# Kernel optimization log

Measured on AMD Instinct MI355X. Metric: run time of the kernel, lower is better.

Reference implementation:

```python
import jax, jax.numpy as jnp
import numpy as np

NUM_EXPERTS = 8
TOP_K = 2
HIDDEN = 2048
INTER = 1024
B, S = 4, 1024


def setup_inputs() -> dict:
    key = jax.random.key(0)
    ks = jax.random.split(key, 5)
    sx = 1.0 / np.sqrt(HIDDEN)
    si = 1.0 / np.sqrt(INTER)
    return {
        "x": jax.random.normal(ks[0], (B, S, HIDDEN), dtype=jnp.float32),
        # router gate: Linear(hidden -> num_experts), weight stored [E, H] (torch convention)
        "gate_w": jax.random.normal(ks[1], (NUM_EXPERTS, HIDDEN), dtype=jnp.float32) * sx,
        # stacked expert weights: gate/up [E, I, H], down [E, H, I]
        "gate_proj_w": jax.random.normal(ks[2], (NUM_EXPERTS, INTER, HIDDEN), dtype=jnp.float32) * sx,
        "up_proj_w": jax.random.normal(ks[3], (NUM_EXPERTS, INTER, HIDDEN), dtype=jnp.float32) * sx,
        "down_proj_w": jax.random.normal(ks[4], (NUM_EXPERTS, HIDDEN, INTER), dtype=jnp.float32) * si,
    }


def _moe_forward(x, gate_w, gate_proj_w, up_proj_w, down_proj_w):
    Bx, Sx, H = x.shape
    T = Bx * Sx
    h = x.reshape(T, H)
    # --- routing (Qwen3: softmax in fp32, top-k, renormalize) ---
    router_logits = h @ gate_w.T                                   # [T, E]
    probs = jax.nn.softmax(router_logits.astype(jnp.float32), axis=-1)
    top_vals, top_idx = jax.lax.top_k(probs, TOP_K)                # [T, K]
    top_vals = top_vals / jnp.sum(top_vals, axis=-1, keepdims=True)  # norm_topk_prob
    # dense routing weights [T, E]: zero for unselected experts
    rw = jnp.zeros((T, NUM_EXPERTS), dtype=jnp.float32)
    rw = rw.at[jnp.arange(T)[:, None], top_idx].add(top_vals)
    rw = rw.astype(h.dtype)
    # --- SwiGLU experts, computed densely and masked by routing weights ---
    g = jnp.einsum('th,eih->tei', h, gate_proj_w)                  # [T, E, I]
    u = jnp.einsum('th,eih->tei', h, up_proj_w)                    # [T, E, I]
    a = jax.nn.silu(g) * u                                         # [T, E, I]
    out_e = jnp.einsum('tei,ehi->teh', a, down_proj_w)             # [T, E, H]
    out = jnp.einsum('te,teh->th', rw, out_e)                      # [T, H]
    return out.reshape(Bx, Sx, H)


def reference(x, gate_w, gate_proj_w, up_proj_w, down_proj_w):
    return _moe_forward(x, gate_w, gate_proj_w, up_proj_w, down_proj_w)
```

## Files before the change

### kernel.cpp

```cpp
#include <hip/hip_runtime.h>
#include <hip/hip_bf16.h>

#define NUM_EXPERTS 8
#define HIDDEN 2048
#define INTER 1024
#define T_TOKENS 4096

#define BK 32
#define GU_BM 64
#define GU_BN 128
#define DN_BM 64
#define DN_BN 128

typedef __attribute__((ext_vector_type(8))) short short8;
typedef __attribute__((ext_vector_type(4))) float f32x4;

__device__ __forceinline__ ushort f2bf(float f) {
    __hip_bfloat16 h = __float2bfloat16(f);
    return *reinterpret_cast<ushort*>(&h);
}

__device__ __forceinline__ void load_lds16(const void* g, void* lds) {
    __builtin_amdgcn_global_load_lds(
        (const __attribute__((address_space(1))) void*)g,
        (__attribute__((address_space(3))) void*)lds, 16, 0, 0);
}

__global__ __launch_bounds__(256) void cvt_bf16(const float* __restrict__ in,
                                                ushort* __restrict__ out, int n4) {
    int i = blockIdx.x * 256 + threadIdx.x;
    int stride = gridDim.x * 256;
    for (; i < n4; i += stride) {
        float4 v = reinterpret_cast<const float4*>(in)[i];
        ushort4 o;
        o.x = f2bf(v.x); o.y = f2bf(v.y); o.z = f2bf(v.z); o.w = f2bf(v.w);
        reinterpret_cast<ushort4*>(out)[i] = o;
    }
}

__global__ __launch_bounds__(256) void moe_router(const float* __restrict__ x,
                                                  const float* __restrict__ gw,
                                                  int* __restrict__ top_idx,
                                                  float* __restrict__ top_w,
                                                  int* __restrict__ counts) {
    int wid = threadIdx.x >> 6;
    int lane = threadIdx.x & 63;
    int t = blockIdx.x * 4 + wid;
    if (t >= T_TOKENS) return;
    const float* xt = x + (size_t)t * HIDDEN;
    float acc[NUM_EXPERTS];
#pragma unroll
    for (int e = 0; e < NUM_EXPERTS; e++) acc[e] = 0.f;
    for (int h = lane; h < HIDDEN; h += 64) {
        float xv = xt[h];
#pragma unroll
        for (int e = 0; e < NUM_EXPERTS; e++)
            acc[e] = fmaf(xv, gw[e * HIDDEN + h], acc[e]);
    }
#pragma unroll
    for (int e = 0; e < NUM_EXPERTS; e++) {
#pragma unroll
        for (int off = 32; off > 0; off >>= 1)
            acc[e] += __shfl_xor(acc[e], off);
    }
    if (lane == 0) {
        int i1 = 0; float l1 = acc[0];
#pragma unroll
        for (int e = 1; e < NUM_EXPERTS; e++)
            if (acc[e] > l1) { l1 = acc[e]; i1 = e; }
        int i2 = -1; float l2 = -3.4e38f;
#pragma unroll
        for (int e = 0; e < NUM_EXPERTS; e++)
            if (e != i1 && acc[e] > l2) { l2 = acc[e]; i2 = e; }
        float w2 = __expf(l2 - l1);
        float denom = 1.f + w2;
        top_idx[t * 2 + 0] = i1;
        top_idx[t * 2 + 1] = i2;
        top_w[t * 2 + 0] = 1.f / denom;
        top_w[t * 2 + 1] = w2 / denom;
        atomicAdd(&counts[i1], 1);
        atomicAdd(&counts[i2], 1);
    }
}

__global__ void moe_offsets(const int* __restrict__ counts,
                            int* __restrict__ ebase, int* __restrict__ cursor) {
    if (threadIdx.x == 0 && blockIdx.x == 0) {
        int s = 0;
        for (int e = 0; e < NUM_EXPERTS; e++) {
            ebase[e] = s; cursor[e] = s; s += counts[e];
        }
    }
}

__global__ __launch_bounds__(256) void moe_scatter(const int* __restrict__ top_idx,
                                                   const float* __restrict__ top_w,
                                                   int* __restrict__ cursor,
                                                   int* __restrict__ slot_tok,
                                                   float* __restrict__ slot_w) {
    int t = blockIdx.x * 256 + threadIdx.x;
    if (t >= T_TOKENS) return;
#pragma unroll
    for (int k = 0; k < 2; k++) {
        int e = top_idx[t * 2 + k];
        int pos = atomicAdd(&cursor[e], 1);
        slot_tok[pos] = t;
        slot_w[pos] = top_w[t * 2 + k];
    }
}

__global__ __launch_bounds__(256, 4) void moe_gateup(const ushort* __restrict__ xb,
                                                     const ushort* __restrict__ wgb,
                                                     const ushort* __restrict__ wub,
                                                     const int* __restrict__ slot_tok,
                                                     const int* __restrict__ ebase,
                                                     const int* __restrict__ ecnt,
                                                     ushort* __restrict__ act) {
    __shared__ ushort ldsA[2][GU_BM * BK];
    __shared__ ushort ldsG[2][GU_BN * BK];
    __shared__ ushort ldsU[2][GU_BN * BK];

    const int wg = blockIdx.x;
    const int wgid = (wg & 7) * 512 + (wg >> 3);
    const int e = wgid >> 9;
    const int rem = wgid & 511;
    const int bm = rem & 63;
    const int bn = rem >> 6;

    const int cnt = ecnt[e];
    if (bm * GU_BM >= cnt) return;
    const int b0 = ebase[e];

    const int tid = threadIdx.x;
    const int lane = tid & 63;
    const int wid = tid >> 6;
    const int wr = wid >> 1, wc = wid & 1;

    const int r = tid >> 2, cs = tid & 3;
    const int scl = (cs ^ ((r >> 1) & 3)) * 8;
    const int ar = bm * GU_BM + r;
    const int tok = slot_tok[b0 + ((ar < cnt) ? ar : (cnt - 1))];
    const ushort* pA = xb + (size_t)tok * HIDDEN + scl;
    const size_t wrow0 = (size_t)e * INTER + (size_t)(bn * GU_BN + r);
    const ushort* pG0 = wgb + wrow0 * HIDDEN + scl;
    const ushort* pG1 = pG0 + (size_t)64 * HIDDEN;
    const ushort* pU0 = wub + wrow0 * HIDDEN + scl;
    const ushort* pU1 = pU0 + (size_t)64 * HIDDEN;

    const int fr = lane & 15;
    const int colsw = (((lane >> 4) ^ ((fr >> 1) & 3)) * 8);

    f32x4 accg[2][4] = {};
    f32x4 accu[2][4] = {};

#define GU_STAGE(buf, t)                                              \
    do {                                                              \
        const int _o = (t) * BK;                                      \
        load_lds16(pA + _o,  &ldsA[buf][tid * 8]);                    \
        load_lds16(pG0 + _o, &ldsG[buf][tid * 8]);                    \
        load_lds16(pG1 + _o, &ldsG[buf][2048 + tid * 8]);             \
        load_lds16(pU0 + _o, &ldsU[buf][tid * 8]);                    \
        load_lds16(pU1 + _o, &ldsU[buf][2048 + tid * 8]);             \
    } while (0)

#define GU_FRAGS_MFMA(cur)                                            \
    do {                                                              \
        const ushort* LA = ldsA[cur];                                 \
        const ushort* LG = ldsG[cur];                                 \
        const ushort* LU = ldsU[cur];                                 \
        short8 a[2], bg[4], bu[4];                                    \
        _Pragma("unroll")                                             \
        for (int m = 0; m < 2; m++)                                   \
            a[m] = *(const short8*)(LA + (wr * 32 + m * 16 + fr) * BK + colsw); \
        _Pragma("unroll")                                             \
        for (int n = 0; n < 4; n++) {                                 \
            bg[n] = *(const short8*)(LG + (wc * 64 + n * 16 + fr) * BK + colsw); \
            bu[n] = *(const short8*)(LU + (wc * 64 + n * 16 + fr) * BK + colsw); \
        }                                                             \
        asm volatile("s_waitcnt lgkmcnt(0)" ::: "memory");            \
        asm volatile("s_barrier" ::: "memory");                       \
        if (t + 2 < NT) GU_STAGE(cur, t + 2);                         \
        _Pragma("unroll")                                             \
        for (int m = 0; m < 2; m++) {                                 \
            _Pragma("unroll")                                         \
            for (int n = 0; n < 4; n++) {                             \
                accg[m][n] = __builtin_amdgcn_mfma_f32_16x16x32_bf16(a[m], bg[n], accg[m][n], 0, 0, 0); \
                accu[m][n] = __builtin_amdgcn_mfma_f32_16x16x32_bf16(a[m], bu[n], accu[m][n], 0, 0, 0); \
            }                                                         \
        }                                                             \
    } while (0)

    const int NT = HIDDEN / BK;
    GU_STAGE(0, 0);
    GU_STAGE(1, 1);

    for (int t = 0; t < NT - 1; ++t) {
        asm volatile("s_waitcnt vmcnt(5)" ::: "memory");
        asm volatile("s_barrier" ::: "memory");
        const int cur = t & 1;
        GU_FRAGS_MFMA(cur);
    }
    {
        const int t = NT - 1;
        asm volatile("s_waitcnt vmcnt(0)" ::: "memory");
        asm volatile("s_barrier" ::: "memory");
        const int cur = t & 1;
        GU_FRAGS_MFMA(cur);
    }
#undef GU_FRAGS_MFMA
#undef GU_STAGE

#pragma unroll
    for (int m = 0; m < 2; m++) {
#pragma unroll
        for (int rr = 0; rr < 4; rr++) {
            int row = bm * GU_BM + wr * 32 + m * 16 + (lane >> 4) * 4 + rr;
            if (row < cnt) {
                size_t arow = (size_t)(b0 + row) * INTER;
#pragma unroll
                for (int n = 0; n < 4; n++) {
                    int col = bn * GU_BN + wc * 64 + n * 16 + fr;
                    float g = accg[m][n][rr];
                    float u = accu[m][n][rr];
                    float s = g / (1.f + __expf(-g));
                    act[arow + col] = f2bf(s * u);
                }
            }
        }
    }
}

__global__ __launch_bounds__(256, 6) void moe_down(const ushort* __restrict__ act,
                                                   const ushort* __restrict__ wdb,
                                                   const int* __restrict__ slot_tok,
                                                   const float* __restrict__ slot_w,
                                                   const int* __restrict__ ebase,
                                                   const int* __restrict__ ecnt,
                                                   float* __restrict__ out) {
    __shared__ ushort ldsA[2][DN_BM * BK];
    __shared__ ushort ldsB[2][DN_BN * BK];

    const int wg = blockIdx.x;
    const int wgid = (wg & 7) * 1024 + (wg >> 3);
    const int e = wgid >> 10;
    const int rem = wgid & 1023;
    const int bm = rem & 63;
    const int bn = rem >> 6;

    const int cnt = ecnt[e];
    if (bm * DN_BM >= cnt) return;
    const int b0 = ebase[e];

    const int tid = threadIdx.x;
    const int lane = tid & 63;
    const int wid = tid >> 6;
    const int wr = wid >> 1, wc = wid & 1;

    const int r = tid >> 2, cs = tid & 3;
    const int scl = (cs ^ ((r >> 1) & 3)) * 8;
    const int ar = bm * DN_BM + r;
    const int sr = b0 + ((ar < cnt) ? ar : (cnt - 1));
    const ushort* pA = act + (size_t)sr * INTER + scl;
    const size_t wrow = (size_t)e * HIDDEN + (size_t)(bn * DN_BN + r);
    const ushort* pB0 = wdb + wrow * INTER + scl;
    const ushort* pB1 = pB0 + (size_t)64 * INTER;

    const int fr = lane & 15;
    const int colsw = (((lane >> 4) ^ ((fr >> 1) & 3)) * 8);

    f32x4 acc[2][4] = {};

#define DN_STAGE(buf, t)                                              \
    do {                                                              \
        const int _o = (t) * BK;                                      \
        load_lds16(pA + _o,  &ldsA[buf][tid * 8]);                    \
        load_lds16(pB0 + _o, &ldsB[buf][tid * 8]);                    \
        load_lds16(pB1 + _o, &ldsB[buf][2048 + tid * 8]);             \
    } while (0)

#define DN_FRAGS_MFMA(cur)                                            \
    do {                                                              \
        const ushort* LA = ldsA[cur];                                 \
        const ushort* LB = ldsB[cur];                                 \
        short8 a[2], b[4];                                            \
        _Pragma("unroll")                                             \
        for (int m = 0; m < 2; m++)                                   \
            a[m] = *(const short8*)(LA + (wr * 32 + m * 16 + fr) * BK + colsw); \
        _Pragma("unroll")                                             \
        for (int n = 0; n < 4; n++)                                   \
            b[n] = *(const short8*)(LB + (wc * 64 + n * 16 + fr) * BK + colsw); \
        asm volatile("s_waitcnt lgkmcnt(0)" ::: "memory");            \
        asm volatile("s_barrier" ::: "memory");                       \
        if (t + 2 < NT) DN_STAGE(cur, t + 2);                         \
        _Pragma("unroll")                                             \
        for (int m = 0; m < 2; m++) {                                 \
            _Pragma("unroll")                                         \
            for (int n = 0; n < 4; n++)                               \
                acc[m][n] = __builtin_amdgcn_mfma_f32_16x16x32_bf16(a[m], b[n], acc[m][n], 0, 0, 0); \
        }                                                             \
    } while (0)

    const int NT = INTER / BK;
    DN_STAGE(0, 0);
    DN_STAGE(1, 1);

    for (int t = 0; t < NT - 1; ++t) {
        asm volatile("s_waitcnt vmcnt(3)" ::: "memory");
        asm volatile("s_barrier" ::: "memory");
        const int cur = t & 1;
        DN_FRAGS_MFMA(cur);
    }
    {
        const int t = NT - 1;
        asm volatile("s_waitcnt vmcnt(0)" ::: "memory");
        asm volatile("s_barrier" ::: "memory");
        const int cur = t & 1;
        DN_FRAGS_MFMA(cur);
    }
#undef DN_FRAGS_MFMA
#undef DN_STAGE

#pragma unroll
    for (int m = 0; m < 2; m++) {
#pragma unroll
        for (int rr = 0; rr < 4; rr++) {
            int row = bm * DN_BM + wr * 32 + m * 16 + (lane >> 4) * 4 + rr;
            if (row < cnt) {
                int slot = b0 + row;
                int tok = slot_tok[slot];
                float w = slot_w[slot];
                float* orow = out + (size_t)tok * HIDDEN;
#pragma unroll
                for (int n = 0; n < 4; n++) {
                    int col = bn * DN_BN + wc * 64 + n * 16 + fr;
                    atomicAdd(&orow[col], acc[m][n][rr] * w);
                }
            }
        }
    }
}

extern "C" void kernel_launch(void* const* d_in, const int* in_sizes, int n_in,
                              void* d_out, int out_size, void* d_ws, size_t ws_size,
                              hipStream_t stream) {
    const float* x  = (const float*)d_in[0];
    const float* gw = (const float*)d_in[1];
    const float* wg = (const float*)d_in[2];
    const float* wu = (const float*)d_in[3];
    const float* wd = (const float*)d_in[4];
    float* out = (float*)d_out;

    char* ws = (char*)d_ws;
    ushort* xb  = (ushort*)(ws);
    ushort* wgb = (ushort*)(ws + 16777216);
    ushort* wub = (ushort*)(ws + 16777216 + 33554432);
    ushort* wdb = (ushort*)(ws + 16777216 + 2u * 33554432);
    ushort* act = (ushort*)(ws + 16777216 + 3u * 33554432);
    char* p = ws + 2u * 16777216 + 3u * 33554432;
    int*   top_idx  = (int*)p;   p += 32768;
    float* top_w    = (float*)p; p += 32768;
    int*   slot_tok = (int*)p;   p += 32768;
    float* slot_w   = (float*)p; p += 32768;
    int*   counts   = (int*)p;   p += 128;
    int*   ebase    = (int*)p;   p += 128;
    int*   cursor   = (int*)p;   p += 128;

    hipMemsetAsync(counts, 0, 128, stream);
    hipMemsetAsync(d_out, 0, (size_t)out_size * sizeof(float), stream);

    cvt_bf16<<<1024, 256, 0, stream>>>(x,  xb,  (T_TOKENS * HIDDEN) / 4);
    cvt_bf16<<<1024, 256, 0, stream>>>(wg, wgb, (NUM_EXPERTS * INTER * HIDDEN) / 4);
    cvt_bf16<<<1024, 256, 0, stream>>>(wu, wub, (NUM_EXPERTS * INTER * HIDDEN) / 4);
    cvt_bf16<<<1024, 256, 0, stream>>>(wd, wdb, (NUM_EXPERTS * HIDDEN * INTER) / 4);

    moe_router<<<T_TOKENS / 4, 256, 0, stream>>>(x, gw, top_idx, top_w, counts);
    moe_offsets<<<1, 64, 0, stream>>>(counts, ebase, cursor);
    moe_scatter<<<(T_TOKENS + 255) / 256, 256, 0, stream>>>(top_idx, top_w, cursor, slot_tok, slot_w);

    moe_gateup<<<4096, 256, 0, stream>>>(xb, wgb, wub, slot_tok, ebase, counts, act);
    moe_down<<<8192, 256, 0, stream>>>(act, wdb, slot_tok, slot_w, ebase, counts, out);
}
```

Baseline: 617.4 us.

## Replace atomic scatter-add in down projection with per-slot stores and gather

The down-projection kernel now writes unweighted per-slot results to a workspace buffer with plain stores instead of weighted atomicAdds into the output. A new gather kernel combines each token's two expert rows using the routing weights, and the output memset is dropped. The scatter kernel records an inverse slot map for this gather. The fp32-to-bf16 conversion is also widened to 8 elements per thread. This trades atomic contention for roughly 96MB of extra memory traffic and one more kernel launch.

```diff
diff --git a/kernel.cpp b/kernel.cpp
--- a/kernel.cpp
+++ b/kernel.cpp
@@ -13,6 +13,7 @@
 #define DN_BN 128
 
 typedef __attribute__((ext_vector_type(8))) short short8;
+typedef __attribute__((ext_vector_type(8))) unsigned short ushort8_t;
 typedef __attribute__((ext_vector_type(4))) float f32x4;
 
 __device__ __forceinline__ ushort f2bf(float f) {
@@ -27,14 +28,16 @@
 }
 
 __global__ __launch_bounds__(256) void cvt_bf16(const float* __restrict__ in,
-                                                ushort* __restrict__ out, int n4) {
+                                                ushort* __restrict__ out, int n8) {
     int i = blockIdx.x * 256 + threadIdx.x;
     int stride = gridDim.x * 256;
-    for (; i < n4; i += stride) {
-        float4 v = reinterpret_cast<const float4*>(in)[i];
-        ushort4 o;
-        o.x = f2bf(v.x); o.y = f2bf(v.y); o.z = f2bf(v.z); o.w = f2bf(v.w);
-        reinterpret_cast<ushort4*>(out)[i] = o;
+    for (; i < n8; i += stride) {
+        const float4* p = (const float4*)in + 2 * (size_t)i;
+        float4 a = p[0], b = p[1];
+        ushort8_t o;
+        o[0] = f2bf(a.x); o[1] = f2bf(a.y); o[2] = f2bf(a.z); o[3] = f2bf(a.w);
+        o[4] = f2bf(b.x); o[5] = f2bf(b.y); o[6] = f2bf(b.z); o[7] = f2bf(b.w);
+        *((ushort8_t*)out + i) = o;
     }
 }
 
@@ -94,10 +97,9 @@
 }
 
 __global__ __launch_bounds__(256) void moe_scatter(const int* __restrict__ top_idx,
-                                                   const float* __restrict__ top_w,
                                                    int* __restrict__ cursor,
                                                    int* __restrict__ slot_tok,
-                                                   float* __restrict__ slot_w) {
+                                                   int* __restrict__ inv_slot) {
     int t = blockIdx.x * 256 + threadIdx.x;
     if (t >= T_TOKENS) return;
 #pragma unroll
@@ -105,7 +107,7 @@
         int e = top_idx[t * 2 + k];
         int pos = atomicAdd(&cursor[e], 1);
         slot_tok[pos] = t;
-        slot_w[pos] = top_w[t * 2 + k];
+        inv_slot[t * 2 + k] = pos;
     }
 }
 
@@ -232,11 +234,9 @@
 
 __global__ __launch_bounds__(256, 6) void moe_down(const ushort* __restrict__ act,
                                                    const ushort* __restrict__ wdb,
-                                                   const int* __restrict__ slot_tok,
-                                                   const float* __restrict__ slot_w,
                                                    const int* __restrict__ ebase,
                                                    const int* __restrict__ ecnt,
-                                                   float* __restrict__ out) {
+                                                   float* __restrict__ out_e) {
     __shared__ ushort ldsA[2][DN_BM * BK];
     __shared__ ushort ldsB[2][DN_BN * BK];
 
@@ -326,17 +326,36 @@
         for (int rr = 0; rr < 4; rr++) {
             int row = bm * DN_BM + wr * 32 + m * 16 + (lane >> 4) * 4 + rr;
             if (row < cnt) {
-                int slot = b0 + row;
-                int tok = slot_tok[slot];
-                float w = slot_w[slot];
-                float* orow = out + (size_t)tok * HIDDEN;
+                float* orow = out_e + (size_t)(b0 + row) * HIDDEN;
 #pragma unroll
                 for (int n = 0; n < 4; n++) {
                     int col = bn * DN_BN + wc * 64 + n * 16 + fr;
-                    atomicAdd(&orow[col], acc[m][n][rr] * w);
+                    orow[col] = acc[m][n][rr];
                 }
             }
         }
+    }
+}
+
+__global__ __launch_bounds__(256) void moe_gather(const float* __restrict__ out_e,
+                                                  const int* __restrict__ inv_slot,
+                                                  const float* __restrict__ top_w,
+                                                  float* __restrict__ out) {
+    int t = blockIdx.x;
+    int c = threadIdx.x * 8;
+    int s0 = inv_slot[t * 2 + 0], s1 = inv_slot[t * 2 + 1];
+    float w0 = top_w[t * 2 + 0], w1 = top_w[t * 2 + 1];
+    const float4* r0 = (const float4*)(out_e + (size_t)s0 * HIDDEN + c);
+    const float4* r1 = (const float4*)(out_e + (size_t)s1 * HIDDEN + c);
+    float4* po = (float4*)(out + (size_t)t * HIDDEN + c);
+#pragma unroll
+    for (int j = 0; j < 2; j++) {
+        float4 a = r0[j], b = r1[j], o;
+        o.x = w0 * a.x + w1 * b.x;
+        o.y = w0 * a.y + w1 * b.y;
+        o.z = w0 * a.z + w1 * b.z;
+        o.w = w0 * a.w + w1 * b.w;
+        po[j] = o;
     }
 }
 
@@ -352,31 +371,32 @@
 
     char* ws = (char*)d_ws;
     ushort* xb  = (ushort*)(ws);
-    ushort* wgb = (ushort*)(ws + 16777216);
-    ushort* wub = (ushort*)(ws + 16777216 + 33554432);
-    ushort* wdb = (ushort*)(ws + 16777216 + 2u * 33554432);
-    ushort* act = (ushort*)(ws + 16777216 + 3u * 33554432);
-    char* p = ws + 2u * 16777216 + 3u * 33554432;
+    ushort* wgb = (ushort*)(ws + (16u << 20));
+    ushort* wub = (ushort*)(ws + (48u << 20));
+    ushort* wdb = (ushort*)(ws + (80u << 20));
+    ushort* act = (ushort*)(ws + (112u << 20));
+    float* out_e = (float*)(ws);
+    char* p = ws + (128u << 20);
     int*   top_idx  = (int*)p;   p += 32768;
     float* top_w    = (float*)p; p += 32768;
     int*   slot_tok = (int*)p;   p += 32768;
-    float* slot_w   = (float*)p; p += 32768;
+    int*   inv_slot = (int*)p;   p += 32768;
     int*   counts   = (int*)p;   p += 128;
     int*   ebase    = (int*)p;   p += 128;
     int*   cursor   = (int*)p;   p += 128;
 
     hipMemsetAsync(counts, 0, 128, stream);
-    hipMemsetAsync(d_out, 0, (size_t)out_size * sizeof(float), stream);
-
-    cvt_bf16<<<1024, 256, 0, stream>>>(x,  xb,  (T_TOKENS * HIDDEN) / 4);
-    cvt_bf16<<<1024, 256, 0, stream>>>(wg, wgb, (NUM_EXPERTS * INTER * HIDDEN) / 4);
-    cvt_bf16<<<1024, 256, 0, stream>>>(wu, wub, (NUM_EXPERTS * INTER * HIDDEN) / 4);
-    cvt_bf16<<<1024, 256, 0, stream>>>(wd, wdb, (NUM_EXPERTS * HIDDEN * INTER) / 4);
+
+    cvt_bf16<<<1024, 256, 0, stream>>>(x,  xb,  (T_TOKENS * HIDDEN) / 8);
+    cvt_bf16<<<1024, 256, 0, stream>>>(wg, wgb, (NUM_EXPERTS * INTER * HIDDEN) / 8);
+    cvt_bf16<<<1024, 256, 0, stream>>>(wu, wub, (NUM_EXPERTS * INTER * HIDDEN) / 8);
+    cvt_bf16<<<1024, 256, 0, stream>>>(wd, wdb, (NUM_EXPERTS * HIDDEN * INTER) / 8);
 
     moe_router<<<T_TOKENS / 4, 256, 0, stream>>>(x, gw, top_idx, top_w, counts);
     moe_offsets<<<1, 64, 0, stream>>>(counts, ebase, cursor);
-    moe_scatter<<<(T_TOKENS + 255) / 256, 256, 0, stream>>>(top_idx, top_w, cursor, slot_tok, slot_w);
+    moe_scatter<<<(T_TOKENS + 255) / 256, 256, 0, stream>>>(top_idx, cursor, slot_tok, inv_slot);
 
     moe_gateup<<<4096, 256, 0, stream>>>(xb, wgb, wub, slot_tok, ebase, counts, act);
-    moe_down<<<8192, 256, 0, stream>>>(act, wdb, slot_tok, slot_w, ebase, counts, out);
-}
+    moe_down<<<8192, 256, 0, stream>>>(act, wdb, ebase, counts, out_e);
+    moe_gather<<<T_TOKENS, 256, 0, stream>>>(out_e, inv_slot, top_w, out);
+}
```

After: 600.7 us. 1.03x faster.
